# Kernel tuning notes

Hardware: AMD Instinct MI355X
Metric: run time of the kernel (lower is better)

## Reference

```python
import jax, jax.numpy as jnp
import numpy as np

B, S, D = 2, 2048, 1024
H = 16
DK = D // H
SCALE = 1.0 / np.sqrt(DK)

def setup_inputs() -> dict:
    key = jax.random.key(0)
    ks = jax.random.split(key, 11)
    std = 1.0 / np.sqrt(D)
    return {
        "query": jax.random.normal(ks[0], (B, S, D), jnp.float32),
        "key":   jax.random.normal(ks[1], (B, S, D), jnp.float32),
        "value": jax.random.normal(ks[2], (B, S, D), jnp.float32),
        "Wq": jax.random.normal(ks[3], (D, H * DK), jnp.float32) * std,
        "bq": jnp.zeros((H * DK,), jnp.float32),
        "Wk": jax.random.normal(ks[4], (D, H * DK), jnp.float32) * std,
        "bk": jnp.zeros((H * DK,), jnp.float32),
        "Wv": jax.random.normal(ks[5], (D, H * DK), jnp.float32) * std,
        "bv": jnp.zeros((H * DK,), jnp.float32),
        "Wo": jax.random.normal(ks[6], (D, D), jnp.float32) * std,
        "bo": jnp.zeros((D,), jnp.float32),
    }

def reference(query, key, value, Wq, bq, Wk, bk, Wv, bv, Wo, bo):
    b, s, _ = query.shape
    # projections -> [b, s, h, d_k]
    q = (query @ Wq + bq).reshape(b, s, H, DK)
    k = (key   @ Wk + bk).reshape(b, s, H, DK)
    v = (value @ Wv + bv).reshape(b, s, H, DK)
    # scores [b, i, j, h]
    scores = jnp.einsum('bihd,bjhd->bijh', q, k) * SCALE
    attn = jax.nn.softmax(scores, axis=2)  # softmax over key dim j
    # dropout rate 0.0 (eval mode) -> identity
    x = jnp.einsum('bijh,bjhd->bihd', attn, v).reshape(b, s, H * DK)
    return x @ Wo + bo
```

## Files before the change

### kernel.cpp

```cpp
#include <hip/hip_runtime.h>
#include <hip/hip_bf16.h>
#include <math.h>
#include <stdint.h>

constexpr int Bb = 2, Ss = 2048, Dd = 1024, Hh = 16;
constexpr int Mm = Bb * Ss;
constexpr int Nn = Dd;
constexpr int Kk = Dd;
constexpr float QSCALE = 0.125f * 1.44269504088896340736f;

typedef unsigned short ushort_t;
typedef __attribute__((ext_vector_type(8))) short bf16x8;
typedef __attribute__((ext_vector_type(4))) float f32x4;

#if __has_builtin(__builtin_amdgcn_exp2f)
#define EXP2F(x) __builtin_amdgcn_exp2f(x)
#else
#define EXP2F(x) exp2f(x)
#endif

__device__ __forceinline__ ushort_t f2bf(float f) {
  union { float f; unsigned u; } v; v.f = f;
  return (ushort_t)((v.u + 0x7fff + ((v.u >> 16) & 1)) >> 16);
}

__device__ __forceinline__ void load16_lds(const void* g, void* l) {
  __builtin_amdgcn_global_load_lds(
      (const __attribute__((address_space(1))) void*)(uintptr_t)g,
      (__attribute__((address_space(3))) void*)(uint32_t)(uintptr_t)l, 16, 0, 0);
}

__global__ __launch_bounds__(256) void prep(
    const float* __restrict__ q, const float* __restrict__ k,
    const float* __restrict__ v, ushort_t* __restrict__ qkvb,
    const float* __restrict__ Wq, const float* __restrict__ Wk,
    const float* __restrict__ Wv, const float* __restrict__ Wo,
    ushort_t* __restrict__ Wt) {
  const int bid = blockIdx.x;
  const int tid = threadIdx.x;
  if (bid < 12288) {
    const int z = bid >> 12, xi = bid & 4095;
    const float* src = (z == 0) ? q : (z == 1) ? k : v;
    ushort_t* dst = qkvb + (size_t)z * Mm * Kk;
    const size_t idx = ((size_t)xi * 256 + tid) * 4;
    const float4 val = *(const float4*)(src + idx);
    ushort4 o;
    o.x = f2bf(val.x); o.y = f2bf(val.y); o.z = f2bf(val.z); o.w = f2bf(val.w);
    *(ushort4*)(dst + idx) = o;
    return;
  }
  const int bid2 = bid - 12288;
  const int z = bid2 >> 8, rem = bid2 & 255;
  const float* W = (z == 0) ? Wq : (z == 1) ? Wk : (z == 2) ? Wv : Wo;
  ushort_t* out = Wt + (size_t)z * Kk * Nn;
  __shared__ float t[64][65];
  const int n0 = (rem & 15) * 64, k0 = (rem >> 4) * 64;
  const int lr = tid >> 4, lc = (tid & 15) * 4;
#pragma unroll
  for (int i = 0; i < 4; i++) {
    const int r = lr + i * 16;
    const float4 vv = *(const float4*)(W + (size_t)(k0 + r) * Nn + n0 + lc);
    t[r][lc] = vv.x; t[r][lc + 1] = vv.y; t[r][lc + 2] = vv.z; t[r][lc + 3] = vv.w;
  }
  __syncthreads();
  const int n = tid >> 2, kc = (tid & 3) * 16;
  ushort_t tmp[16];
#pragma unroll
  for (int j = 0; j < 16; j++) tmp[j] = f2bf(t[kc + j][n]);
  ushort_t* op = out + (size_t)(n0 + n) * Kk + k0 + kc;
  ((uint4*)op)[0] = ((uint4*)tmp)[0];
  ((uint4*)op)[1] = ((uint4*)tmp)[1];
}

__global__ __launch_bounds__(256) void transpose_v(
    const ushort_t* __restrict__ Vp, ushort_t* __restrict__ Vt) {
  __shared__ ushort_t t[64][68];
  const int tid = threadIdx.x;
  const int s0 = blockIdx.x * 64, h = blockIdx.y, b = blockIdx.z;
  const int lr = tid >> 4, lc = (tid & 15) * 4;
#pragma unroll
  for (int i = 0; i < 4; i++) {
    const int r = lr + i * 16;
    const ushort4 v =
        *(const ushort4*)(Vp + (size_t)(b * Ss + s0 + r) * Dd + h * 64 + lc);
    *(ushort4*)&t[r][lc] = v;
  }
  __syncthreads();
  const int d = tid >> 2, sc = (tid & 3) * 16;
  ushort_t tmp[16];
#pragma unroll
  for (int j = 0; j < 16; j++) tmp[j] = t[sc + j][d];
  ushort_t* op = Vt + ((size_t)b * Dd + h * 64 + d) * Ss + s0 + sc;
  ((uint4*)op)[0] = ((uint4*)tmp)[0];
  ((uint4*)op)[1] = ((uint4*)tmp)[1];
}

template <int BN, bool OUT_BF16>
__global__ __launch_bounds__(256) void gemm_mfma(
    const ushort_t* __restrict__ Abase, size_t a_stride,
    const ushort_t* __restrict__ Wbase, size_t w_stride,
    const float* __restrict__ bias0, const float* __restrict__ bias1,
    const float* __restrict__ bias2, void* __restrict__ Cbase, size_t c_stride,
    float scale_z0) {
  constexpr int BM = 128, BK = 32;
  constexpr int WM = (BN == 128) ? 64 : 32;
  constexpr int MT_ = WM / 16, NT_ = 4;
  __shared__ ushort_t As[BM * BK];
  __shared__ ushort_t Bs[BN * BK];
  const int tid = threadIdx.x, lane = tid & 63, wid = tid >> 6;
  const int z = blockIdx.z;
  const ushort_t* A = Abase + (size_t)z * a_stride;
  const ushort_t* Wt = Wbase + (size_t)z * w_stride;
  const float* bias = (z == 0) ? bias0 : (z == 1) ? bias1 : bias2;
  const float sc = (z == 0) ? scale_z0 : 1.0f;
  const int m0 = blockIdx.y * BM, n0 = blockIdx.x * BN;
  const int wm = (BN == 128) ? (wid >> 1) * 64 : wid * 32;
  const int wn = (BN == 128) ? (wid & 1) * 64 : 0;
  const int quad = lane >> 4, r16 = lane & 15;
  const int srow = lane >> 2;
  const int scol = (lane & 3) * 8;

  f32x4 acc[MT_][NT_];
#pragma unroll
  for (int m = 0; m < MT_; m++)
#pragma unroll
    for (int n = 0; n < NT_; n++) acc[m][n] = f32x4{0.f, 0.f, 0.f, 0.f};

  for (int k0 = 0; k0 < Kk; k0 += BK) {
    __syncthreads();
#pragma unroll
    for (int i = 0; i < BM / 64; i++) {
      const int I = wid * (BM / 64) + i;
      load16_lds(A + (size_t)(m0 + I * 16 + srow) * Kk + k0 + scol, As + I * 512);
    }
#pragma unroll
    for (int i = 0; i < BN / 64; i++) {
      const int I = wid * (BN / 64) + i;
      load16_lds(Wt + (size_t)(n0 + I * 16 + srow) * Kk + k0 + scol, Bs + I * 512);
    }
    __syncthreads();
    bf16x8 af[MT_], bfr[NT_];
#pragma unroll
    for (int m = 0; m < MT_; m++)
      af[m] = *(const bf16x8*)(As + (wm + m * 16 + r16) * BK + quad * 8);
#pragma unroll
    for (int n = 0; n < NT_; n++)
      bfr[n] = *(const bf16x8*)(Bs + (wn + n * 16 + r16) * BK + quad * 8);
#pragma unroll
    for (int m = 0; m < MT_; m++)
#pragma unroll
      for (int n = 0; n < NT_; n++)
        acc[m][n] =
            __builtin_amdgcn_mfma_f32_16x16x32_bf16(af[m], bfr[n], acc[m][n], 0, 0, 0);
  }

#pragma unroll
  for (int m = 0; m < MT_; m++) {
#pragma unroll
    for (int n = 0; n < NT_; n++) {
      const int gc = n0 + wn + n * 16 + r16;
      const float bv = bias[gc];
#pragma unroll
      for (int r = 0; r < 4; r++) {
        const int gr = m0 + wm + m * 16 + quad * 4 + r;
        const float v = (acc[m][n][r] + bv) * sc;
        if (OUT_BF16)
          ((ushort_t*)Cbase)[(size_t)z * c_stride + (size_t)gr * Nn + gc] = f2bf(v);
        else
          ((float*)Cbase)[(size_t)z * c_stride + (size_t)gr * Nn + gc] = v;
      }
    }
  }
}

__global__ __launch_bounds__(256, 3) void flash_mfma(
    const ushort_t* __restrict__ Qp, const ushort_t* __restrict__ Kp,
    const ushort_t* __restrict__ Vt, ushort_t* __restrict__ Xp) {
  __shared__ float red[2 * 64 * 68];

  const int tid = threadIdx.x, lane = tid & 63, wid = tid >> 6;
  const int lid = blockIdx.x + (blockIdx.y << 5) + (blockIdx.z << 9);
  const int swzb = ((lid & 7) << 7) + (lid >> 3);
  const int qt = swzb & 31, h = (swzb >> 5) & 15, b = swzb >> 9;
  const int quad = lane >> 4, r16 = lane & 15;

  const ushort_t* Qg = Qp + ((size_t)(b * Ss + qt * 64)) * Dd + h * 64;
  const ushort_t* Kg = Kp + ((size_t)b * Ss) * Dd + h * 64;
  const ushort_t* Vg = Vt + ((size_t)b * Dd + h * 64) * Ss;

  const ushort_t* Kw = Kg + (size_t)(wid * 16 + r16) * Dd + quad * 8;
  const ushort_t* Vw = Vg + (size_t)r16 * Ss + wid * 16 + quad * 4;

  bf16x8 qf[2][4];
#pragma unroll
  for (int n = 0; n < 4; n++)
#pragma unroll
    for (int ks = 0; ks < 2; ks++)
      qf[ks][n] = *(const bf16x8*)(Qg + (size_t)(n * 16 + r16) * Dd + ks * 32 + quad * 8);

  f32x4 acc[4][4];
#pragma unroll
  for (int mt = 0; mt < 4; mt++)
#pragma unroll
    for (int n = 0; n < 4; n++) acc[mt][n] = f32x4{0.f, 0.f, 0.f, 0.f};
  float rsn[4] = {0.f, 0.f, 0.f, 0.f};

  for (int kt2 = 0; kt2 < Ss / 128; kt2++) {
    const size_t offA = (size_t)(kt2 * 128) * Dd;
    const size_t offB = offA + (size_t)64 * Dd;
    const int colA = kt2 * 128, colB = colA + 64;

    bf16x8 kfA0 = *(const bf16x8*)(Kw + offA);
    bf16x8 kfA1 = *(const bf16x8*)(Kw + offA + 32);
    bf16x8 kfB0 = *(const bf16x8*)(Kw + offB);
    bf16x8 kfB1 = *(const bf16x8*)(Kw + offB + 32);
    uint2 vA[4];
#pragma unroll
    for (int mt = 0; mt < 4; mt++)
      vA[mt] = *(const uint2*)(Vw + (size_t)(mt * 16) * Ss + colA);

    f32x4 sacc[4];
#pragma unroll
    for (int n = 0; n < 4; n++) sacc[n] = f32x4{0.f, 0.f, 0.f, 0.f};
    __builtin_amdgcn_s_setprio(1);
#pragma unroll
    for (int n = 0; n < 4; n++)
      sacc[n] = __builtin_amdgcn_mfma_f32_16x16x32_bf16(kfA0, qf[0][n], sacc[n], 0, 0, 0);
#pragma unroll
    for (int n = 0; n < 4; n++)
      sacc[n] = __builtin_amdgcn_mfma_f32_16x16x32_bf16(kfA1, qf[1][n], sacc[n], 0, 0, 0);
    __builtin_amdgcn_s_setprio(0);

    uint2 pA[4];
#pragma unroll
    for (int n = 0; n < 4; n++) {
      const float p0 = EXP2F(sacc[n][0]), p1 = EXP2F(sacc[n][1]);
      const float p2 = EXP2F(sacc[n][2]), p3 = EXP2F(sacc[n][3]);
      rsn[n] += (p0 + p1) + (p2 + p3);
      union { __hip_bfloat162 hh; unsigned u; } lo, hi;
      lo.hh = __float22bfloat162_rn(make_float2(p0, p1));
      hi.hh = __float22bfloat162_rn(make_float2(p2, p3));
      pA[n] = make_uint2(lo.u, hi.u);
    }
    uint2 vB[4];
#pragma unroll
    for (int mt = 0; mt < 4; mt++)
      vB[mt] = *(const uint2*)(Vw + (size_t)(mt * 16) * Ss + colB);

#pragma unroll
    for (int n = 0; n < 4; n++) sacc[n] = f32x4{0.f, 0.f, 0.f, 0.f};
    __builtin_amdgcn_s_setprio(1);
#pragma unroll
    for (int n = 0; n < 4; n++)
      sacc[n] = __builtin_amdgcn_mfma_f32_16x16x32_bf16(kfB0, qf[0][n], sacc[n], 0, 0, 0);
#pragma unroll
    for (int n = 0; n < 4; n++)
      sacc[n] = __builtin_amdgcn_mfma_f32_16x16x32_bf16(kfB1, qf[1][n], sacc[n], 0, 0, 0);
    __builtin_amdgcn_s_setprio(0);

    bf16x8 pf[4];
#pragma unroll
    for (int n = 0; n < 4; n++) {
      const float p0 = EXP2F(sacc[n][0]), p1 = EXP2F(sacc[n][1]);
      const float p2 = EXP2F(sacc[n][2]), p3 = EXP2F(sacc[n][3]);
      rsn[n] += (p0 + p1) + (p2 + p3);
      union { __hip_bfloat162 hh; unsigned u; } lo, hi;
      lo.hh = __float22bfloat162_rn(make_float2(p0, p1));
      hi.hh = __float22bfloat162_rn(make_float2(p2, p3));
      union { uint4 u; bf16x8 v; } pk;
      pk.u = make_uint4(pA[n].x, pA[n].y, lo.u, hi.u);
      pf[n] = pk.v;
    }

    __builtin_amdgcn_s_setprio(1);
#pragma unroll
    for (int mt = 0; mt < 4; mt++) {
      union { uint4 u; bf16x8 v; } vk;
      vk.u = make_uint4(vA[mt].x, vA[mt].y, vB[mt].x, vB[mt].y);
#pragma unroll
      for (int n = 0; n < 4; n++)
        acc[mt][n] = __builtin_amdgcn_mfma_f32_16x16x32_bf16(vk.v, pf[n], acc[mt][n], 0, 0, 0);
    }
    __builtin_amdgcn_s_setprio(0);
  }

#pragma unroll
  for (int n = 0; n < 4; n++) {
    float r = rsn[n];
    r += __shfl_xor(r, 16, 64);
    r += __shfl_xor(r, 32, 64);
    rsn[n] = r;
  }

  __syncthreads();
  if (wid & 2) {
    float* p = red + (size_t)(wid & 1) * (64 * 68) + (size_t)lane * 68;
#pragma unroll
    for (int mt = 0; mt < 4; mt++)
#pragma unroll
      for (int n = 0; n < 4; n++)
        *(f32x4*)(p + (mt * 4 + n) * 4) = acc[mt][n];
    p[64] = rsn[0]; p[65] = rsn[1]; p[66] = rsn[2]; p[67] = rsn[3];
  }
  __syncthreads();
  if (!(wid & 2)) {
    const float* p = red + (size_t)wid * (64 * 68) + (size_t)lane * 68;
#pragma unroll
    for (int mt = 0; mt < 4; mt++)
#pragma unroll
      for (int n = 0; n < 4; n++)
        acc[mt][n] += *(const f32x4*)(p + (mt * 4 + n) * 4);
    rsn[0] += p[64]; rsn[1] += p[65]; rsn[2] += p[66]; rsn[3] += p[67];
  }
  __syncthreads();
  if (wid == 1) {
    float* p = red + (size_t)lane * 68;
#pragma unroll
    for (int mt = 0; mt < 4; mt++)
#pragma unroll
      for (int n = 0; n < 4; n++)
        *(f32x4*)(p + (mt * 4 + n) * 4) = acc[mt][n];
    p[64] = rsn[0]; p[65] = rsn[1]; p[66] = rsn[2]; p[67] = rsn[3];
  }
  __syncthreads();
  if (wid == 0) {
    const float* p = red + (size_t)lane * 68;
#pragma unroll
    for (int mt = 0; mt < 4; mt++)
#pragma unroll
      for (int n = 0; n < 4; n++)
        acc[mt][n] += *(const f32x4*)(p + (mt * 4 + n) * 4);
    rsn[0] += p[64]; rsn[1] += p[65]; rsn[2] += p[66]; rsn[3] += p[67];
    float inv[4];
#pragma unroll
    for (int n = 0; n < 4; n++) inv[n] = 1.0f / rsn[n];
#pragma unroll
    for (int mt = 0; mt < 4; mt++) {
#pragma unroll
      for (int n = 0; n < 4; n++) {
        ushort4 o;
        o.x = f2bf(acc[mt][n][0] * inv[n]);
        o.y = f2bf(acc[mt][n][1] * inv[n]);
        o.z = f2bf(acc[mt][n][2] * inv[n]);
        o.w = f2bf(acc[mt][n][3] * inv[n]);
        *(ushort4*)(Xp + (size_t)(b * Ss + qt * 64 + n * 16 + r16) * Dd +
                    h * 64 + mt * 16 + quad * 4) = o;
      }
    }
  }
}

extern "C" void kernel_launch(void* const* d_in, const int* in_sizes, int n_in,
                              void* d_out, int out_size, void* d_ws,
                              size_t ws_size, hipStream_t stream) {
  const float* q  = (const float*)d_in[0];
  const float* k  = (const float*)d_in[1];
  const float* v  = (const float*)d_in[2];
  const float* Wq = (const float*)d_in[3];
  const float* bq = (const float*)d_in[4];
  const float* Wk = (const float*)d_in[5];
  const float* bk = (const float*)d_in[6];
  const float* Wv = (const float*)d_in[7];
  const float* bv = (const float*)d_in[8];
  const float* Wo = (const float*)d_in[9];
  const float* bo = (const float*)d_in[10];

  ushort_t* ws = (ushort_t*)d_ws;
  const size_t MD = (size_t)Mm * Kk;
  const size_t KN = (size_t)Kk * Nn;
  ushort_t* qkvb = ws;
  ushort_t* Wt   = ws + 3 * MD;
  ushort_t* QKVp = Wt + 4 * KN;
  ushort_t* Vtp  = QKVp + 3 * MD;
  ushort_t* Xp   = qkvb;

  prep<<<dim3(13312), 256, 0, stream>>>(q, k, v, qkvb, Wq, Wk, Wv, Wo, Wt);
  gemm_mfma<128, true><<<dim3(Nn / 128, Mm / 128, 3), 256, 0, stream>>>(
      qkvb, MD, Wt, KN, bq, bk, bv, QKVp, MD, QSCALE);
  transpose_v<<<dim3(Ss / 64, Hh, Bb), 256, 0, stream>>>(QKVp + 2 * MD, Vtp);
  flash_mfma<<<dim3(Ss / 64, Hh, Bb), 256, 0, stream>>>(QKVp, QKVp + MD, Vtp, Xp);
  gemm_mfma<64, false><<<dim3(Nn / 64, Mm / 128, 1), 256, 0, stream>>>(
      Xp, 0, Wt + 3 * KN, 0, bo, bo, bo, d_out, 0, 1.0f);
}
```

Baseline: 276.3 us.

## Software-pipeline K prefetch in flash attention loop and raise occupancy bound

Restructures the attention inner loop into a two-tile ping-pong so that K fragments for the next tile are loaded while the current tile is computed, and V loads are grouped up front. It also raises the launch-bounds minimum from 3 to 4 blocks per CU. The intent is to hide global-memory latency for K/V loads. The extra live registers for the prefetched buffers combined with the tighter register budget from the higher occupancy target risk spilling.

```diff
diff --git a/kernel.cpp b/kernel.cpp
--- a/kernel.cpp
+++ b/kernel.cpp
@@ -173,7 +173,7 @@
   }
 }
 
-__global__ __launch_bounds__(256, 3) void flash_mfma(
+__global__ __launch_bounds__(256, 4) void flash_mfma(
     const ushort_t* __restrict__ Qp, const ushort_t* __restrict__ Kp,
     const ushort_t* __restrict__ Vt, ushort_t* __restrict__ Xp) {
   __shared__ float red[2 * 64 * 68];
@@ -205,30 +205,34 @@
     for (int n = 0; n < 4; n++) acc[mt][n] = f32x4{0.f, 0.f, 0.f, 0.f};
   float rsn[4] = {0.f, 0.f, 0.f, 0.f};
 
-  for (int kt2 = 0; kt2 < Ss / 128; kt2++) {
+  auto issueK = [&](int kt2, bf16x8 (&kf)[4]) {
     const size_t offA = (size_t)(kt2 * 128) * Dd;
     const size_t offB = offA + (size_t)64 * Dd;
+    kf[0] = *(const bf16x8*)(Kw + offA);
+    kf[1] = *(const bf16x8*)(Kw + offA + 32);
+    kf[2] = *(const bf16x8*)(Kw + offB);
+    kf[3] = *(const bf16x8*)(Kw + offB + 32);
+  };
+  auto issueV = [&](int kt2, uint2 (&vv)[8]) {
     const int colA = kt2 * 128, colB = colA + 64;
-
-    bf16x8 kfA0 = *(const bf16x8*)(Kw + offA);
-    bf16x8 kfA1 = *(const bf16x8*)(Kw + offA + 32);
-    bf16x8 kfB0 = *(const bf16x8*)(Kw + offB);
-    bf16x8 kfB1 = *(const bf16x8*)(Kw + offB + 32);
-    uint2 vA[4];
-#pragma unroll
-    for (int mt = 0; mt < 4; mt++)
-      vA[mt] = *(const uint2*)(Vw + (size_t)(mt * 16) * Ss + colA);
-
+#pragma unroll
+    for (int mt = 0; mt < 4; mt++) {
+      vv[mt]     = *(const uint2*)(Vw + (size_t)(mt * 16) * Ss + colA);
+      vv[4 + mt] = *(const uint2*)(Vw + (size_t)(mt * 16) * Ss + colB);
+    }
+  };
+
+  auto computeTile = [&](const bf16x8 (&kf)[4], const uint2 (&vv)[8]) {
     f32x4 sacc[4];
 #pragma unroll
     for (int n = 0; n < 4; n++) sacc[n] = f32x4{0.f, 0.f, 0.f, 0.f};
     __builtin_amdgcn_s_setprio(1);
 #pragma unroll
     for (int n = 0; n < 4; n++)
-      sacc[n] = __builtin_amdgcn_mfma_f32_16x16x32_bf16(kfA0, qf[0][n], sacc[n], 0, 0, 0);
+      sacc[n] = __builtin_amdgcn_mfma_f32_16x16x32_bf16(kf[0], qf[0][n], sacc[n], 0, 0, 0);
 #pragma unroll
     for (int n = 0; n < 4; n++)
-      sacc[n] = __builtin_amdgcn_mfma_f32_16x16x32_bf16(kfA1, qf[1][n], sacc[n], 0, 0, 0);
+      sacc[n] = __builtin_amdgcn_mfma_f32_16x16x32_bf16(kf[1], qf[1][n], sacc[n], 0, 0, 0);
     __builtin_amdgcn_s_setprio(0);
 
     uint2 pA[4];
@@ -242,20 +246,16 @@
       hi.hh = __float22bfloat162_rn(make_float2(p2, p3));
       pA[n] = make_uint2(lo.u, hi.u);
     }
-    uint2 vB[4];
-#pragma unroll
-    for (int mt = 0; mt < 4; mt++)
-      vB[mt] = *(const uint2*)(Vw + (size_t)(mt * 16) * Ss + colB);
 
 #pragma unroll
     for (int n = 0; n < 4; n++) sacc[n] = f32x4{0.f, 0.f, 0.f, 0.f};
     __builtin_amdgcn_s_setprio(1);
 #pragma unroll
     for (int n = 0; n < 4; n++)
-      sacc[n] = __builtin_amdgcn_mfma_f32_16x16x32_bf16(kfB0, qf[0][n], sacc[n], 0, 0, 0);
+      sacc[n] = __builtin_amdgcn_mfma_f32_16x16x32_bf16(kf[2], qf[0][n], sacc[n], 0, 0, 0);
 #pragma unroll
     for (int n = 0; n < 4; n++)
-      sacc[n] = __builtin_amdgcn_mfma_f32_16x16x32_bf16(kfB1, qf[1][n], sacc[n], 0, 0, 0);
+      sacc[n] = __builtin_amdgcn_mfma_f32_16x16x32_bf16(kf[3], qf[1][n], sacc[n], 0, 0, 0);
     __builtin_amdgcn_s_setprio(0);
 
     bf16x8 pf[4];
@@ -276,12 +276,24 @@
 #pragma unroll
     for (int mt = 0; mt < 4; mt++) {
       union { uint4 u; bf16x8 v; } vk;
-      vk.u = make_uint4(vA[mt].x, vA[mt].y, vB[mt].x, vB[mt].y);
+      vk.u = make_uint4(vv[mt].x, vv[mt].y, vv[4 + mt].x, vv[4 + mt].y);
 #pragma unroll
       for (int n = 0; n < 4; n++)
         acc[mt][n] = __builtin_amdgcn_mfma_f32_16x16x32_bf16(vk.v, pf[n], acc[mt][n], 0, 0, 0);
     }
     __builtin_amdgcn_s_setprio(0);
+  };
+
+  bf16x8 kfA[4], kfB[4];
+  uint2 vvA[8], vvB[8];
+  issueK(0, kfA);
+  for (int kt2 = 0; kt2 < Ss / 128; kt2 += 2) {
+    issueV(kt2, vvA);
+    issueK(kt2 + 1, kfB);
+    computeTile(kfA, vvA);
+    issueV(kt2 + 1, vvB);
+    if (kt2 + 2 < Ss / 128) issueK(kt2 + 2, kfA);
+    computeTile(kfB, vvB);
   }
 
 #pragma unroll
```

Result: slower. 521.2 us (+88.6%).

## Double-buffer K tiles through swizzled LDS in flash attention loop

Applied to the files above, without the earlier changes.

The K tile for each 128-key step is now staged into a double-buffered, XOR-swizzled shared-memory region with direct global-to-LDS loads. The next tile is prefetched while the current one is used, so K fetch latency overlaps with the MFMA and exp work instead of stalling it. The V loads for both halves are hoisted to the top of the iteration. The LDS region is reused for the final reduction buffer. The cost is a block-wide barrier every iteration and a dependence on vmcnt ordering for the staged data being visible before it is read.

```diff
diff --git a/kernel.cpp b/kernel.cpp
--- a/kernel.cpp
+++ b/kernel.cpp
@@ -176,19 +176,22 @@
 __global__ __launch_bounds__(256, 3) void flash_mfma(
     const ushort_t* __restrict__ Qp, const ushort_t* __restrict__ Kp,
     const ushort_t* __restrict__ Vt, ushort_t* __restrict__ Xp) {
-  __shared__ float red[2 * 64 * 68];
+  __shared__ __align__(16) char smem[34816];
+  ushort_t* KsU = (ushort_t*)smem;
+  float* red = (float*)smem;
 
   const int tid = threadIdx.x, lane = tid & 63, wid = tid >> 6;
   const int lid = blockIdx.x + (blockIdx.y << 5) + (blockIdx.z << 9);
   const int swzb = ((lid & 7) << 7) + (lid >> 3);
   const int qt = swzb & 31, h = (swzb >> 5) & 15, b = swzb >> 9;
   const int quad = lane >> 4, r16 = lane & 15;
+  const int row8 = lane >> 3;
+  const int colsw = ((lane & 7) ^ row8) * 8;
 
   const ushort_t* Qg = Qp + ((size_t)(b * Ss + qt * 64)) * Dd + h * 64;
   const ushort_t* Kg = Kp + ((size_t)b * Ss) * Dd + h * 64;
   const ushort_t* Vg = Vt + ((size_t)b * Dd + h * 64) * Ss;
 
-  const ushort_t* Kw = Kg + (size_t)(wid * 16 + r16) * Dd + quad * 8;
   const ushort_t* Vw = Vg + (size_t)r16 * Ss + wid * 16 + quad * 4;
 
   bf16x8 qf[2][4];
@@ -198,6 +201,11 @@
     for (int ks = 0; ks < 2; ks++)
       qf[ks][n] = *(const bf16x8*)(Qg + (size_t)(n * 16 + r16) * Dd + ks * 32 + quad * 8);
 
+  const uint32_t kbaseA = (uint32_t)(wid * 16 + r16) * 64;
+  const uint32_t kbaseB = kbaseA + 64 * 64;
+  const uint32_t ko0 = (uint32_t)(((0 * 4 + quad) ^ (r16 & 7)) << 3);
+  const uint32_t ko1 = (uint32_t)(((1 * 4 + quad) ^ (r16 & 7)) << 3);
+
   f32x4 acc[4][4];
 #pragma unroll
   for (int mt = 0; mt < 4; mt++)
@@ -205,19 +213,38 @@
     for (int n = 0; n < 4; n++) acc[mt][n] = f32x4{0.f, 0.f, 0.f, 0.f};
   float rsn[4] = {0.f, 0.f, 0.f, 0.f};
 
-  for (int kt2 = 0; kt2 < Ss / 128; kt2++) {
-    const size_t offA = (size_t)(kt2 * 128) * Dd;
-    const size_t offB = offA + (size_t)64 * Dd;
-    const int colA = kt2 * 128, colB = colA + 64;
-
-    bf16x8 kfA0 = *(const bf16x8*)(Kw + offA);
-    bf16x8 kfA1 = *(const bf16x8*)(Kw + offA + 32);
-    bf16x8 kfB0 = *(const bf16x8*)(Kw + offB);
-    bf16x8 kfB1 = *(const bf16x8*)(Kw + offB + 32);
-    uint2 vA[4];
-#pragma unroll
-    for (int mt = 0; mt < 4; mt++)
+  constexpr int NT = Ss / 128;
+
+  auto stageK = [&](int t, int bsel) {
+#pragma unroll
+    for (int i = 0; i < 4; i++) {
+      const int I = wid * 4 + i;
+      load16_lds(Kg + (size_t)(t * 128 + I * 8 + row8) * Dd + colsw,
+                 KsU + bsel * 8192 + I * 512);
+    }
+  };
+
+  stageK(0, 0);
+  asm volatile("s_waitcnt vmcnt(0)" ::: "memory");
+  __syncthreads();
+
+  for (int t = 0; t < NT; t++) {
+    const int cur = t & 1;
+    if (t + 1 < NT) stageK(t + 1, cur ^ 1);
+
+    const int colA = t * 128, colB = colA + 64;
+    uint2 vA[4], vB[4];
+#pragma unroll
+    for (int mt = 0; mt < 4; mt++) {
       vA[mt] = *(const uint2*)(Vw + (size_t)(mt * 16) * Ss + colA);
+      vB[mt] = *(const uint2*)(Vw + (size_t)(mt * 16) * Ss + colB);
+    }
+
+    const ushort_t* Kc = KsU + cur * 8192;
+    const bf16x8 kfA0 = *(const bf16x8*)(Kc + kbaseA + ko0);
+    const bf16x8 kfA1 = *(const bf16x8*)(Kc + kbaseA + ko1);
+    const bf16x8 kfB0 = *(const bf16x8*)(Kc + kbaseB + ko0);
+    const bf16x8 kfB1 = *(const bf16x8*)(Kc + kbaseB + ko1);
 
     f32x4 sacc[4];
 #pragma unroll
@@ -242,10 +269,6 @@
       hi.hh = __float22bfloat162_rn(make_float2(p2, p3));
       pA[n] = make_uint2(lo.u, hi.u);
     }
-    uint2 vB[4];
-#pragma unroll
-    for (int mt = 0; mt < 4; mt++)
-      vB[mt] = *(const uint2*)(Vw + (size_t)(mt * 16) * Ss + colB);
 
 #pragma unroll
     for (int n = 0; n < 4; n++) sacc[n] = f32x4{0.f, 0.f, 0.f, 0.f};
@@ -282,6 +305,8 @@
         acc[mt][n] = __builtin_amdgcn_mfma_f32_16x16x32_bf16(vk.v, pf[n], acc[mt][n], 0, 0, 0);
     }
     __builtin_amdgcn_s_setprio(0);
+
+    __syncthreads();
   }
 
 #pragma unroll
```

Result: slower. 302.4 us (+9.4%).

## Stage K/V tiles through double-buffered swizzled LDS with async global-to-LDS loads

Applied to the files above, without the earlier changes.

The attention kernel stops loading K and V fragments straight from global memory in each wave. Each pair of 64-key tiles is now copied into a double-buffered, XOR-swizzled LDS area with direct global-to-LDS loads. The next pair is prefetched while the current one is consumed, using vmcnt waits and barriers to keep the buffers in step. The goal is better coalescing of the scattered V loads and hiding global-memory latency behind the MFMA work. In exchange it uses 64KB of shared memory, lowers the occupancy target from 3 to 2 blocks, and adds two barriers per iteration.

```diff
diff --git a/kernel.cpp b/kernel.cpp
--- a/kernel.cpp
+++ b/kernel.cpp
@@ -173,24 +173,27 @@
   }
 }
 
-__global__ __launch_bounds__(256, 3) void flash_mfma(
+__global__ __launch_bounds__(256, 2) void flash_mfma(
     const ushort_t* __restrict__ Qp, const ushort_t* __restrict__ Kp,
     const ushort_t* __restrict__ Vt, ushort_t* __restrict__ Xp) {
-  __shared__ float red[2 * 64 * 68];
+  __shared__ __align__(16) char smem[65536];
+  ushort_t* KsU = (ushort_t*)smem;
+  ushort_t* VtsU = KsU + 16384;
+  float* red = (float*)smem;
 
   const int tid = threadIdx.x, lane = tid & 63, wid = tid >> 6;
   const int lid = blockIdx.x + (blockIdx.y << 5) + (blockIdx.z << 9);
   const int swzb = ((lid & 7) << 7) + (lid >> 3);
   const int qt = swzb & 31, h = (swzb >> 5) & 15, b = swzb >> 9;
   const int quad = lane >> 4, r16 = lane & 15;
+  const int row8 = lane >> 3;
+  const int colsw = ((lane & 7) ^ row8) * 8;
+  const int swz = r16 & 7;
 
   const ushort_t* Qg = Qp + ((size_t)(b * Ss + qt * 64)) * Dd + h * 64;
   const ushort_t* Kg = Kp + ((size_t)b * Ss) * Dd + h * 64;
   const ushort_t* Vg = Vt + ((size_t)b * Dd + h * 64) * Ss;
 
-  const ushort_t* Kw = Kg + (size_t)(wid * 16 + r16) * Dd + quad * 8;
-  const ushort_t* Vw = Vg + (size_t)r16 * Ss + wid * 16 + quad * 4;
-
   bf16x8 qf[2][4];
 #pragma unroll
   for (int n = 0; n < 4; n++)
@@ -198,6 +201,12 @@
     for (int ks = 0; ks < 2; ks++)
       qf[ks][n] = *(const bf16x8*)(Qg + (size_t)(n * 16 + r16) * Dd + ks * 32 + quad * 8);
 
+  const uint32_t kbase = (uint32_t)(wid * 16 + r16) * 64;
+  const uint32_t ko0 = (uint32_t)((quad ^ swz) << 3);
+  const uint32_t ko1 = (uint32_t)(((4 + quad) ^ swz) << 3);
+  const int vG = wid * 2 + (quad >> 1);
+  const uint32_t vcol = (uint32_t)(((vG ^ swz) << 3) + (quad & 1) * 4);
+
   f32x4 acc[4][4];
 #pragma unroll
   for (int mt = 0; mt < 4; mt++)
@@ -205,19 +214,41 @@
     for (int n = 0; n < 4; n++) acc[mt][n] = f32x4{0.f, 0.f, 0.f, 0.f};
   float rsn[4] = {0.f, 0.f, 0.f, 0.f};
 
-  for (int kt2 = 0; kt2 < Ss / 128; kt2++) {
-    const size_t offA = (size_t)(kt2 * 128) * Dd;
-    const size_t offB = offA + (size_t)64 * Dd;
-    const int colA = kt2 * 128, colB = colA + 64;
-
-    bf16x8 kfA0 = *(const bf16x8*)(Kw + offA);
-    bf16x8 kfA1 = *(const bf16x8*)(Kw + offA + 32);
-    bf16x8 kfB0 = *(const bf16x8*)(Kw + offB);
-    bf16x8 kfB1 = *(const bf16x8*)(Kw + offB + 32);
-    uint2 vA[4];
-#pragma unroll
-    for (int mt = 0; mt < 4; mt++)
-      vA[mt] = *(const uint2*)(Vw + (size_t)(mt * 16) * Ss + colA);
+  constexpr int NP = Ss / 128;
+
+  auto stage64 = [&](int t64, ushort_t* Kd, ushort_t* Vd) {
+#pragma unroll
+    for (int i = 0; i < 2; i++) {
+      const int I = wid * 2 + i;
+      load16_lds(Kg + (size_t)(t64 * 64 + I * 8 + row8) * Dd + colsw, Kd + I * 512);
+      load16_lds(Vg + (size_t)(I * 8 + row8) * Ss + t64 * 64 + colsw, Vd + I * 512);
+    }
+  };
+  auto stagePair = [&](int p, int bsel) {
+    stage64(p * 2 + 0, KsU + bsel * 8192, VtsU + bsel * 8192);
+    stage64(p * 2 + 1, KsU + bsel * 8192 + 4096, VtsU + bsel * 8192 + 4096);
+  };
+
+  stagePair(0, 0);
+  asm volatile("s_waitcnt vmcnt(8)" ::: "memory");
+
+  for (int p = 0; p < NP; p++) {
+    const int cur = p & 1;
+    if (p + 1 < NP) {
+      stagePair(p + 1, cur ^ 1);
+      asm volatile("s_waitcnt vmcnt(8)\n\ts_barrier" ::: "memory");
+    } else {
+      asm volatile("s_waitcnt vmcnt(0)\n\ts_barrier" ::: "memory");
+    }
+    const ushort_t* KcA = KsU + cur * 8192;
+    const ushort_t* KcB = KcA + 4096;
+    const ushort_t* VcA = VtsU + cur * 8192;
+    const ushort_t* VcB = VcA + 4096;
+
+    const bf16x8 kfA0 = *(const bf16x8*)(KcA + kbase + ko0);
+    const bf16x8 kfA1 = *(const bf16x8*)(KcA + kbase + ko1);
+    const bf16x8 kfB0 = *(const bf16x8*)(KcB + kbase + ko0);
+    const bf16x8 kfB1 = *(const bf16x8*)(KcB + kbase + ko1);
 
     f32x4 sacc[4];
 #pragma unroll
@@ -242,10 +273,6 @@
       hi.hh = __float22bfloat162_rn(make_float2(p2, p3));
       pA[n] = make_uint2(lo.u, hi.u);
     }
-    uint2 vB[4];
-#pragma unroll
-    for (int mt = 0; mt < 4; mt++)
-      vB[mt] = *(const uint2*)(Vw + (size_t)(mt * 16) * Ss + colB);
 
 #pragma unroll
     for (int n = 0; n < 4; n++) sacc[n] = f32x4{0.f, 0.f, 0.f, 0.f};
@@ -275,13 +302,17 @@
     __builtin_amdgcn_s_setprio(1);
 #pragma unroll
     for (int mt = 0; mt < 4; mt++) {
+      const uint2 vA = *(const uint2*)(VcA + (uint32_t)(mt * 16 + r16) * 64 + vcol);
+      const uint2 vB = *(const uint2*)(VcB + (uint32_t)(mt * 16 + r16) * 64 + vcol);
       union { uint4 u; bf16x8 v; } vk;
-      vk.u = make_uint4(vA[mt].x, vA[mt].y, vB[mt].x, vB[mt].y);
+      vk.u = make_uint4(vA.x, vA.y, vB.x, vB.y);
 #pragma unroll
       for (int n = 0; n < 4; n++)
         acc[mt][n] = __builtin_amdgcn_mfma_f32_16x16x32_bf16(vk.v, pf[n], acc[mt][n], 0, 0, 0);
     }
     __builtin_amdgcn_s_setprio(0);
+
+    asm volatile("s_barrier" ::: "memory");
   }
 
 #pragma unroll
```

Measured after the change: 233.3 us. -15.6%, faster.
